# Kernel tuning notes

Hardware: AMD Instinct MI355X
Metric: run time of the kernel (lower is better)

Reference implementation:

```python
import jax, jax.numpy as jnp
import numpy as np

DIM = 512
HEADS = 8
AGENT = 49
POOL = 7  # int(sqrt(49))
EPS = 1e-5  # BatchNorm eps


def _adaptive_avg_pool(x, out_hw):
    # torch AdaptiveAvgPool2d semantics: bin i covers [floor(i*H/out), ceil((i+1)*H/out))
    B, C, H, W = x.shape
    cs = jnp.cumsum(jnp.cumsum(x, axis=2), axis=3)
    cs = jnp.pad(cs, ((0, 0), (0, 0), (1, 0), (1, 0)))  # integral image, [B,C,H+1,W+1]
    hs = np.floor(np.arange(out_hw) * H / out_hw).astype(np.int32)
    he = np.ceil((np.arange(out_hw) + 1) * H / out_hw).astype(np.int32)
    ws = np.floor(np.arange(out_hw) * W / out_hw).astype(np.int32)
    we = np.ceil((np.arange(out_hw) + 1) * W / out_hw).astype(np.int32)
    area = ((he - hs)[:, None] * (we - ws)[None, :]).astype(np.float32)
    s = (cs[:, :, he][:, :, :, we] - cs[:, :, hs][:, :, :, we]
         - cs[:, :, he][:, :, :, ws] + cs[:, :, hs][:, :, :, ws])
    return s / area


def setup_inputs() -> dict:
    key = jax.random.key(0)
    ks = jax.random.split(key, 8)
    d = DIM

    def w(k, shape, s=0.02):
        return jax.random.normal(k, shape, jnp.float32) * s

    return {
        "x": jax.random.normal(ks[0], (16, d, 32, 32), jnp.float32),
        "H": 32,
        "W": 32,
        "q_w": w(ks[1], (d, d)),
        "kv_w": w(ks[2], (2 * d, d)),
        "dw_w": w(ks[3], (d, 1, 3, 3), 0.1),   # depthwise 3x3, groups=d
        "dw_b": jnp.zeros((d,), jnp.float32),
        "bn_gamma": jnp.ones((d,), jnp.float32),
        "bn_beta": jnp.zeros((d,), jnp.float32),
        "bn_mean": jnp.zeros((d,), jnp.float32),
        "bn_var": jnp.ones((d,), jnp.float32),
        "pw_w": w(ks[4], (d, d, 1, 1)),          # pointwise 1x1 conv
        "pw_b": jnp.zeros((d,), jnp.float32),
        "proj_w": w(ks[5], (d, d)),
        "proj_b": jnp.zeros((d,), jnp.float32),
        "enh1_w": w(ks[6], (d, d)),
        "enh1_b": jnp.zeros((d,), jnp.float32),
        "enh2_w": w(ks[7], (d, d)),
        "enh2_b": jnp.zeros((d,), jnp.float32),
    }


def reference(x, H, W, q_w, kv_w, dw_w, dw_b, bn_gamma, bn_beta, bn_mean, bn_var,
              pw_w, pw_b, proj_w, proj_b, enh1_w, enh1_b, enh2_w, enh2_b):
    B, C, H, W = x.shape  # torch re-reads sizes from x
    N = H * W
    hd = C // HEADS
    scale = hd ** -0.5
    dn = ('NCHW', 'OIHW', 'NCHW')

    x_flat = x.reshape(B, C, N).transpose(0, 2, 1)            # [B,N,C]
    q = (x_flat @ q_w.T).reshape(B, N, HEADS, hd).transpose(0, 2, 1, 3)  # [B,h,N,hd]
    kv = (x_flat @ kv_w.T).reshape(B, N, 2, HEADS, hd).transpose(2, 0, 3, 1, 4)
    k, v = kv[0], kv[1]                                        # [B,h,N,hd]

    # agent tokens (faithful raw reshapes as in the torch code)
    a = _adaptive_avg_pool(x, POOL)                            # [B,C,7,7]
    a = a.reshape(B, C, AGENT).transpose(0, 2, 1)              # [B,49,C]
    a = a.reshape(B, C, POOL, POOL)                            # raw reshape (torch bug, kept)
    a = jax.lax.conv_general_dilated(a, dw_w, (1, 1), 'SAME',
                                     feature_group_count=C, dimension_numbers=dn)
    a = a + dw_b[None, :, None, None]
    a = (a - bn_mean[None, :, None, None]) * jax.lax.rsqrt(bn_var + EPS)[None, :, None, None]
    a = a * bn_gamma[None, :, None, None] + bn_beta[None, :, None, None]
    a = jax.nn.relu(a)
    a = jax.lax.conv_general_dilated(a, pw_w, (1, 1), 'SAME', dimension_numbers=dn)
    a = a + pw_b[None, :, None, None]
    a = a.reshape(B, AGENT, C)                                 # raw reshape
    a = a.reshape(B, HEADS, AGENT, hd)                         # raw reshape (torch bug, kept)

    # stage 1: agent <- kv
    agent_attn = jax.nn.softmax(jnp.einsum('bhad,bhnd->bhan', a, k) * scale, axis=-1)
    agg = jnp.einsum('bhan,bhnd->bhad', agent_attn, v)         # [B,h,49,hd]
    # stage 2: q <- agent
    q_attn = jax.nn.softmax(jnp.einsum('bhnd,bhad->bhna', q, a) * scale, axis=-1)
    enh = jnp.einsum('bhna,bhad->bhnd', q_attn, agg)           # [B,h,N,hd]
    enh = enh.transpose(0, 2, 1, 3).reshape(B, N, C)

    x_out = enh @ proj_w.T + proj_b
    out = (jax.nn.relu(x_out @ enh1_w.T + enh1_b) @ enh2_w.T + enh2_b) + x_out
    return out.reshape(B, C, H, W)  # raw reshape as in torch
```

## Files before the change

### kernel.cpp

```cpp
#include <hip/hip_runtime.h>
#include <stdint.h>


typedef float f32x4 __attribute__((ext_vector_type(4)));
typedef short s16x8 __attribute__((ext_vector_type(8)));

typedef __attribute__((address_space(1))) void glob_v;
typedef __attribute__((address_space(3))) void lds_v;
#define GLD16(g, l) \
  __builtin_amdgcn_global_load_lds((glob_v*)(g), (lds_v*)(l), 16, 0, 0)
#define VMCNT(N) asm volatile("s_waitcnt vmcnt(" #N ")" ::: "memory")
#define BAR() __builtin_amdgcn_s_barrier()

__device__ __forceinline__ float bf2f(unsigned short u) {
  union { unsigned int i; float f; } v; v.i = ((unsigned int)u) << 16; return v.f;
}
__device__ __forceinline__ unsigned short f2bf(float f) {
  union { float f; unsigned int i; } v; v.f = f;
  return (unsigned short)((v.i + 0x7FFFu + ((v.i >> 16) & 1u)) >> 16);
}

__constant__ int ws7[7] = {0, 4, 9, 13, 18, 22, 27};
__constant__ int we7[7] = {5, 10, 14, 19, 23, 28, 32};

__global__ __launch_bounds__(256) void k_transpose(const float* __restrict__ x,
                                                   unsigned short* __restrict__ xT,
                                                   float* __restrict__ p_rows) {
  __shared__ float tile[64][65];
  const int b = blockIdx.z, c0 = blockIdx.y * 64, n0 = blockIdx.x * 64;
  const int t = threadIdx.x, tn = t & 63, tg = t >> 6;
#pragma unroll
  for (int i = 0; i < 16; ++i) {
    const int c_l = tg * 16 + i;
    tile[c_l][tn] = x[(b * 512 + c0 + c_l) * 1024 + n0 + tn];
  }
  __syncthreads();
#pragma unroll
  for (int i = 0; i < 16; ++i) {
    const int n_l = tg * 16 + i;
    xT[(b * 1024 + n0 + n_l) * 512 + c0 + tn] = f2bf(tile[tn][n_l]);
  }
  if (t < 128) {
    const int c_l = t >> 1, rw = t & 1;
    const int rowg = blockIdx.x * 2 + rw;
    const float* src = &tile[c_l][rw * 32];
    float* dst = p_rows + ((b * 512 + c0 + c_l) * 32 + rowg) * 8;
#pragma unroll
    for (int jb = 0; jb < 7; ++jb) {
      float s = 0.f;
      for (int cc = ws7[jb]; cc < we7[jb]; ++cc) s += src[cc];
      dst[jb] = s;
    }
  }
}

__global__ __launch_bounds__(256) void k_poolred(const float* __restrict__ p_rows,
                                                 float* __restrict__ p) {
  const int u = blockIdx.x * 256 + threadIdx.x;
  if (u >= 401408) return;
  const int bc = u / 49, ij = u % 49;
  const int i = ij / 7, j = ij % 7;
  float s = 0.f;
  for (int r = ws7[i]; r < we7[i]; ++r) s += p_rows[bc * 256 + r * 8 + j];
  const float area = (float)((we7[i] - ws7[i]) * (we7[j] - ws7[j]));
  p[u] = s / area;
}

__global__ __launch_bounds__(256) void k_weights(
    const float* __restrict__ qw, const float* __restrict__ kvw,
    const float* __restrict__ pjw, const float* __restrict__ w1,
    const float* __restrict__ w2, unsigned short* __restrict__ Wqkv,
    unsigned short* __restrict__ Wpj, unsigned short* __restrict__ W1,
    unsigned short* __restrict__ W2) {
  const int u = blockIdx.x * 256 + threadIdx.x;
  const float* s; unsigned short* d; int su, du;
  if (u < 196608) { d = Wqkv; du = u;
    if (u < 65536) { s = qw; su = u; } else { s = kvw; su = u - 65536; } }
  else if (u < 262144) { s = pjw; su = u - 196608; d = Wpj; du = su; }
  else if (u < 327680) { s = w1; su = u - 262144; d = W1; du = su; }
  else { s = w2; su = u - 327680; d = W2; du = su; }
  const f32x4 val = ((const f32x4*)s)[su];
  uint2 pk;
  pk.x = (unsigned)f2bf(val[0]) | ((unsigned)f2bf(val[1]) << 16);
  pk.y = (unsigned)f2bf(val[2]) | ((unsigned)f2bf(val[3]) << 16);
  ((uint2*)d)[du] = pk;
}

__global__ __launch_bounds__(256) void k_dw(
    const float* __restrict__ p, const float* __restrict__ dww,
    const float* __restrict__ dwb, const float* __restrict__ g,
    const float* __restrict__ be, const float* __restrict__ mean,
    const float* __restrict__ var, float* __restrict__ r) {
  const int t = threadIdx.x, s = t & 63;
  if (s >= 49) return;
  const int bc = blockIdx.x * 4 + (t >> 6);
  const int b = bc >> 9, c = bc & 511;
  const int i = s / 7, j = s % 7;
  float sum = 0.f;
#pragma unroll
  for (int ki = 0; ki < 3; ++ki)
#pragma unroll
    for (int kj = 0; kj < 3; ++kj) {
      const int ii = i + ki - 1, jj = j + kj - 1;
      if (ii < 0 || ii > 6 || jj < 0 || jj > 6) continue;
      const int f = c * 49 + ii * 7 + jj;
      sum += dww[c * 9 + ki * 3 + kj] * p[(b * 512 + (f & 511)) * 49 + (f >> 9)];
    }
  sum += dwb[c];
  sum = (sum - mean[c]) * rsqrtf(var[c] + 1e-5f) * g[c] + be[c];
  r[bc * 49 + s] = fmaxf(sum, 0.f);
}

__global__ __launch_bounds__(256) void k_pw(const float* __restrict__ r,
                                            const float* __restrict__ w,
                                            const float* __restrict__ bias,
                                            float* __restrict__ A) {
  __shared__ float wl[128 * 36];
  __shared__ float rl[128 * 64];
  const int blk = blockIdx.x;
  const int b = blk >> 4, cg = blk & 15;
  const int t = threadIdx.x, wv = t >> 6, lane = t & 63;
  float acc[8];
#pragma unroll
  for (int j = 0; j < 8; ++j) acc[j] = 0.f;
  for (int ch = 0; ch < 4; ++ch) {
    __syncthreads();
#pragma unroll
    for (int u = t; u < 4096; u += 256) {
      const int co = u >> 7, ci = u & 127;
      wl[ci * 36 + co] = w[(cg * 32 + co) * 512 + ch * 128 + ci];
    }
    for (int u = t; u < 6272; u += 256) {
      const int ci = u / 49, s = u % 49;
      rl[ci * 64 + s] = r[b * 25088 + ch * 6272 + u];
    }
    __syncthreads();
#pragma unroll 4
    for (int ci = 0; ci < 128; ++ci) {
      const f32x4 w0 = *(const f32x4*)(wl + ci * 36 + wv * 8);
      const f32x4 w1 = *(const f32x4*)(wl + ci * 36 + wv * 8 + 4);
      const float rv = rl[ci * 64 + lane];
#pragma unroll
      for (int j = 0; j < 4; ++j) { acc[j] += w0[j] * rv; acc[4 + j] += w1[j] * rv; }
    }
  }
  if (lane < 49) {
#pragma unroll
    for (int j = 0; j < 8; ++j) {
      const int co = cg * 32 + wv * 8 + j;
      A[b * 25088 + co * 49 + lane] = acc[j] + bias[co];
    }
  }
}

template <int MODE>
__global__ __launch_bounds__(256) void k_gemm(
    const unsigned short* __restrict__ A, const unsigned short* __restrict__ B,
    unsigned short* __restrict__ oq, unsigned short* __restrict__ ok,
    unsigned short* __restrict__ ov, float* __restrict__ of,
    unsigned short* __restrict__ obf, const float* __restrict__ bias,
    const float* __restrict__ resid, float* __restrict__ dout) {
  __shared__ unsigned short As[3][4096];
  __shared__ unsigned short Bs[3][4096];
  const int t = threadIdx.x;
  constexpr int NB = (MODE == 0) ? 12 : 4;
  constexpr int NWG = NB * 128;
  const int swz = ((int)blockIdx.x & 7) * (NWG >> 3) + ((int)blockIdx.x >> 3);
  const int n0 = (swz % NB) * 128, m0 = (swz / NB) * 128;
  const int w = t >> 6, lane = t & 63;
  const int wr = w >> 1, wc = w & 1, lr = lane & 15, lg = lane >> 4;
  const unsigned short* gA = A + m0 * 512;
  const unsigned short* gB = B + n0 * 512;

  const int s_rp = t >> 3;
  const int s_g = (t & 7) ^ (s_rp & 7);
  const int s_r = (s_rp << 1) | (s_g >> 2);
  const int s_kq = (s_g & 3) * 8;
  auto stage = [&](int cur, int kt) {
    const int ko = kt * 32 + s_kq;
    GLD16(gA + s_r * 512 + ko, As[cur] + w * 512);
    GLD16(gA + (s_r + 64) * 512 + ko, As[cur] + 2048 + w * 512);
    GLD16(gB + s_r * 512 + ko, Bs[cur] + w * 512);
    GLD16(gB + (s_r + 64) * 512 + ko, Bs[cur] + 2048 + w * 512);
  };
  auto ldsw = [&](const unsigned short* hb, int rl, int lgq) -> s16x8 {
    const int rp = rl >> 1;
    const int gs = (((rl & 1) << 2) | lgq) ^ (rp & 7);
    return *(const s16x8*)(hb + rp * 64 + gs * 8);
  };

  f32x4 acc[4][4];
#pragma unroll
  for (int mi = 0; mi < 4; ++mi)
#pragma unroll
    for (int ni = 0; ni < 4; ++ni)
#pragma unroll
      for (int rr = 0; rr < 4; ++rr) acc[mi][ni][rr] = 0.f;

  stage(0, 0);
  stage(1, 1);
  for (int kt = 0; kt < 16; ++kt) {
    const int cur = kt % 3;
    if (kt < 14) {
      stage((kt + 2) % 3, kt + 2);
      VMCNT(8);
    } else if (kt == 14) {
      VMCNT(4);
    } else {
      VMCNT(0);
    }
    BAR();
    const unsigned short* Ah = As[cur] + wr * 2048;
    const unsigned short* Bh = Bs[cur] + wc * 2048;
    s16x8 af[4], bfr[4];
#pragma unroll
    for (int mi = 0; mi < 4; ++mi) af[mi] = ldsw(Ah, mi * 16 + lr, lg);
#pragma unroll
    for (int ni = 0; ni < 4; ++ni) bfr[ni] = ldsw(Bh, ni * 16 + lr, lg);
    __builtin_amdgcn_s_setprio(1);
#pragma unroll
    for (int mi = 0; mi < 4; ++mi)
#pragma unroll
      for (int ni = 0; ni < 4; ++ni)
        acc[mi][ni] = __builtin_amdgcn_mfma_f32_16x16x32_bf16(af[mi], bfr[ni],
                                                              acc[mi][ni], 0, 0, 0);
    __builtin_amdgcn_s_setprio(0);
    BAR();
  }

#pragma unroll
  for (int mi = 0; mi < 4; ++mi)
#pragma unroll
    for (int ni = 0; ni < 4; ++ni)
#pragma unroll
      for (int rr = 0; rr < 4; ++rr) {
        const int gm = m0 + wr * 64 + mi * 16 + lg * 4 + rr;
        const int gn = n0 + wc * 64 + ni * 16 + lr;
        const float val = acc[mi][ni][rr];
        if (MODE == 0) {
          const int b = gm >> 10, n = gm & 1023;
          const int hh = (gn >> 6) & 7, dd = gn & 63;
          const int idx = ((b * 8 + hh) * 1024 + n) * 64 + dd;
          const unsigned short bv = f2bf(val);
          if (gn < 512) oq[idx] = bv;
          else if (gn < 1024) ok[idx] = bv;
          else ov[idx] = bv;
        } else if (MODE == 1) {
          const float v2 = val + bias[gn];
          of[gm * 512 + gn] = v2;
          obf[gm * 512 + gn] = f2bf(v2);
        } else if (MODE == 2) {
          const float v2 = fmaxf(val + bias[gn], 0.f);
          obf[gm * 512 + gn] = f2bf(v2);
        } else {
          dout[gm * 512 + gn] = val + bias[gn] + resid[gm * 512 + gn];
        }
      }
}

__global__ __launch_bounds__(256) void k_aflash(
    const float* __restrict__ Abuf, const unsigned short* __restrict__ kbf,
    const unsigned short* __restrict__ vbf, float* __restrict__ numT,
    float* __restrict__ denG) {
  __shared__ unsigned short A_lds[64 * 72];
  __shared__ unsigned short K_lds[64 * 72];
  __shared__ unsigned short VT_lds[64 * 72];
  __shared__ unsigned short P_lds[64 * 72];
  const int blk = blockIdx.x;
  const int bh = blk >> 2, qtr = blk & 3;
  const int b = bh >> 3, h = bh & 7;
  const int t = threadIdx.x, w = t >> 6, lane = t & 63;
  const int lr = lane & 15, lg = lane >> 4;

  for (int u = t; u < 64 * 72; u += 256) A_lds[u] = 0;
  __syncthreads();
  for (int u = t; u < 3136; u += 256) {
    const int d = u / 49, ag = u % 49;
    A_lds[ag * 72 + d] = f2bf(Abuf[b * 25088 + (h * 64 + d) * 49 + ag]);
  }

  const unsigned short* kbase = kbf + bh * 65536 + qtr * 256 * 64;
  const unsigned short* vbase = vbf + bh * 65536 + qtr * 256 * 64;

  f32x4 num[4];
#pragma unroll
  for (int ni = 0; ni < 4; ++ni)
#pragma unroll
    for (int rr = 0; rr < 4; ++rr) num[ni][rr] = 0.f;
  float den[4] = {0.f, 0.f, 0.f, 0.f};

  for (int c = 0; c < 4; ++c) {
    const int n0 = c * 64;
    __syncthreads();
#pragma unroll
    for (int u = t; u < 512; u += 256) {
      const int rw = u >> 3, qq = u & 7;
      *(s16x8*)(K_lds + rw * 72 + qq * 8) =
          *(const s16x8*)(kbase + (n0 + rw) * 64 + qq * 8);
    }
#pragma unroll
    for (int u = t; u < 512; u += 256) {
      const int n_l = u & 63, qq = u >> 6;
      const s16x8 v = *(const s16x8*)(vbase + (n0 + n_l) * 64 + qq * 8);
#pragma unroll
      for (int j = 0; j < 8; ++j)
        VT_lds[(qq * 8 + j) * 72 + n_l] = (unsigned short)v[j];
    }
    __syncthreads();
    f32x4 s[4];
#pragma unroll
    for (int ni = 0; ni < 4; ++ni)
#pragma unroll
      for (int rr = 0; rr < 4; ++rr) s[ni][rr] = 0.f;
#pragma unroll
    for (int kk = 0; kk < 2; ++kk) {
      const s16x8 afr = *(const s16x8*)(A_lds + (w * 16 + lr) * 72 + kk * 32 + lg * 8);
#pragma unroll
      for (int ni = 0; ni < 4; ++ni) {
        const s16x8 bfr =
            *(const s16x8*)(K_lds + (ni * 16 + lr) * 72 + kk * 32 + lg * 8);
        s[ni] = __builtin_amdgcn_mfma_f32_16x16x32_bf16(afr, bfr, s[ni], 0, 0, 0);
      }
    }
#pragma unroll
    for (int ni = 0; ni < 4; ++ni)
#pragma unroll
      for (int rr = 0; rr < 4; ++rr) {
        const float p = __expf(s[ni][rr] * 0.125f);
        den[rr] += p;
        P_lds[(w * 16 + lg * 4 + rr) * 72 + ni * 16 + lr] = f2bf(p);
      }
#pragma unroll
    for (int kk = 0; kk < 2; ++kk) {
      const s16x8 pa = *(const s16x8*)(P_lds + (w * 16 + lr) * 72 + kk * 32 + lg * 8);
#pragma unroll
      for (int ni = 0; ni < 4; ++ni) {
        const s16x8 vfr =
            *(const s16x8*)(VT_lds + (ni * 16 + lr) * 72 + kk * 32 + lg * 8);
        num[ni] = __builtin_amdgcn_mfma_f32_16x16x32_bf16(pa, vfr, num[ni], 0, 0, 0);
      }
    }
  }
#pragma unroll
  for (int rr = 0; rr < 4; ++rr) {
#pragma unroll
    for (int o = 1; o < 16; o <<= 1) den[rr] += __shfl_xor(den[rr], o, 64);
  }
  const int obase = (qtr * 128 + bh) * 4096;
#pragma unroll
  for (int ni = 0; ni < 4; ++ni)
    *(f32x4*)(numT + obase + (ni * 16 + lr) * 64 + w * 16 + lg * 4) = num[ni];
  if (lr == 0) {
    f32x4 dv;
#pragma unroll
    for (int rr = 0; rr < 4; ++rr) dv[rr] = den[rr];
    *(f32x4*)(denG + (qtr * 128 + bh) * 64 + w * 16 + lg * 4) = dv;
  }
}

__global__ __launch_bounds__(256) void k_attn2(
    const float* __restrict__ Abuf, const float* __restrict__ numT,
    const float* __restrict__ denG, const unsigned short* __restrict__ qbf,
    unsigned short* __restrict__ enh) {
  __shared__ unsigned short A_lds[64 * 72];
  __shared__ unsigned short G_lds[64 * 72];
  __shared__ unsigned short P2_lds[4][64 * 72];
  __shared__ float den_lds[64];
  const int blk = blockIdx.x;
  const int bh = blk >> 2, nq = blk & 3;
  const int b = bh >> 3, h = bh & 7;
  const int t = threadIdx.x, w = t >> 6, lane = t & 63;
  const int lr = lane & 15, lg = lane >> 4;

  if (t < 64)
    den_lds[t] = 1.f / (denG[bh * 64 + t] + denG[8192 + bh * 64 + t] +
                        denG[16384 + bh * 64 + t] + denG[24576 + bh * 64 + t]);
  for (int u = t; u < 64 * 72; u += 256) A_lds[u] = 0;
  __syncthreads();
  for (int u = t; u < 3136; u += 256) {
    const int d = u / 49, ag = u % 49;
    A_lds[ag * 72 + d] = f2bf(Abuf[b * 25088 + (h * 64 + d) * 49 + ag]);
  }
  for (int u = t; u < 4096; u += 256) {
    const int d = u >> 6, ag = u & 63;
    const float v = (numT[bh * 4096 + u] + numT[524288 + bh * 4096 + u] +
                     numT[1048576 + bh * 4096 + u] + numT[1572864 + bh * 4096 + u]) *
                    den_lds[ag];
    G_lds[d * 72 + ag] = f2bf(v);
  }
  __syncthreads();

  const int nbase = nq * 256 + w * 64;
  const unsigned short* qp = qbf + (bh * 1024 + nbase) * 64;
  s16x8 qf[4][2];
#pragma unroll
  for (int mi = 0; mi < 4; ++mi)
#pragma unroll
    for (int kk = 0; kk < 2; ++kk)
      qf[mi][kk] = *(const s16x8*)(qp + (mi * 16 + lr) * 64 + kk * 32 + lg * 8);

  f32x4 L[4][4];
#pragma unroll
  for (int mi = 0; mi < 4; ++mi)
#pragma unroll
    for (int ni = 0; ni < 4; ++ni)
#pragma unroll
      for (int rr = 0; rr < 4; ++rr) L[mi][ni][rr] = 0.f;
#pragma unroll
  for (int kk = 0; kk < 2; ++kk)
#pragma unroll
    for (int ni = 0; ni < 4; ++ni) {
      const s16x8 bfr = *(const s16x8*)(A_lds + (ni * 16 + lr) * 72 + kk * 32 + lg * 8);
#pragma unroll
      for (int mi = 0; mi < 4; ++mi)
        L[mi][ni] = __builtin_amdgcn_mfma_f32_16x16x32_bf16(qf[mi][kk], bfr,
                                                            L[mi][ni], 0, 0, 0);
    }
  unsigned short* pw = P2_lds[w];
#pragma unroll
  for (int mi = 0; mi < 4; ++mi) {
    float ps[4][4];
    float rs[4];
#pragma unroll
    for (int rr = 0; rr < 4; ++rr) rs[rr] = 0.f;
#pragma unroll
    for (int ni = 0; ni < 4; ++ni) {
      const bool valid = (ni < 3) | (lr == 0);
#pragma unroll
      for (int rr = 0; rr < 4; ++rr) {
        const float p = valid ? __expf(L[mi][ni][rr] * 0.125f) : 0.f;
        ps[ni][rr] = p;
        rs[rr] += p;
      }
    }
#pragma unroll
    for (int rr = 0; rr < 4; ++rr) {
#pragma unroll
      for (int o = 1; o < 16; o <<= 1) rs[rr] += __shfl_xor(rs[rr], o, 64);
      rs[rr] = 1.f / rs[rr];
    }
#pragma unroll
    for (int ni = 0; ni < 4; ++ni)
#pragma unroll
      for (int rr = 0; rr < 4; ++rr)
        pw[(mi * 16 + lg * 4 + rr) * 72 + ni * 16 + lr] = f2bf(ps[ni][rr] * rs[rr]);
  }
#pragma unroll
  for (int mi = 0; mi < 4; ++mi) {
    f32x4 e[4];
#pragma unroll
    for (int ni = 0; ni < 4; ++ni)
#pragma unroll
      for (int rr = 0; rr < 4; ++rr) e[ni][rr] = 0.f;
#pragma unroll
    for (int kk = 0; kk < 2; ++kk) {
      const s16x8 pa = *(const s16x8*)(pw + (mi * 16 + lr) * 72 + kk * 32 + lg * 8);
#pragma unroll
      for (int ni = 0; ni < 4; ++ni) {
        const s16x8 gb = *(const s16x8*)(G_lds + (ni * 16 + lr) * 72 + kk * 32 + lg * 8);
        e[ni] = __builtin_amdgcn_mfma_f32_16x16x32_bf16(pa, gb, e[ni], 0, 0, 0);
      }
    }
#pragma unroll
    for (int ni = 0; ni < 4; ++ni)
#pragma unroll
      for (int rr = 0; rr < 4; ++rr) {
        const int n = nbase + mi * 16 + lg * 4 + rr;
        enh[(b * 1024 + n) * 512 + h * 64 + ni * 16 + lr] = f2bf(e[ni][rr]);
      }
  }
}

extern "C" void kernel_launch(void* const* d_in, const int* in_sizes, int n_in,
                              void* d_out, int out_size, void* d_ws, size_t ws_size,
                              hipStream_t stream) {
  const float* x    = (const float*)d_in[0];
  const float* q_w  = (const float*)d_in[3];
  const float* kv_w = (const float*)d_in[4];
  const float* dw_w = (const float*)d_in[5];
  const float* dw_b = (const float*)d_in[6];
  const float* bn_g = (const float*)d_in[7];
  const float* bn_b = (const float*)d_in[8];
  const float* bn_m = (const float*)d_in[9];
  const float* bn_v = (const float*)d_in[10];
  const float* pw_w = (const float*)d_in[11];
  const float* pw_b = (const float*)d_in[12];
  const float* pj_w = (const float*)d_in[13];
  const float* pj_b = (const float*)d_in[14];
  const float* e1_w = (const float*)d_in[15];
  const float* e1_b = (const float*)d_in[16];
  const float* e2_w = (const float*)d_in[17];
  const float* e2_b = (const float*)d_in[18];

  char* base = (char*)d_ws;
  size_t off = 0;
  auto alloc = [&](size_t bytes) -> void* {
    void* r = base + off;
    off += (bytes + 255) & ~(size_t)255;
    return r;
  };
  unsigned short* Wqkv = (unsigned short*)alloc(786432ull * 2);
  unsigned short* Wpj  = (unsigned short*)alloc(262144ull * 2);
  unsigned short* W1   = (unsigned short*)alloc(262144ull * 2);
  unsigned short* W2   = (unsigned short*)alloc(262144ull * 2);
  unsigned short* xT   = (unsigned short*)alloc(8388608ull * 2);
  unsigned short* qb   = (unsigned short*)alloc(8388608ull * 2);
  unsigned short* kb   = (unsigned short*)alloc(8388608ull * 2);
  unsigned short* vb   = (unsigned short*)alloc(8388608ull * 2);
  float* prow = (float*)alloc(2097152ull * 4);
  float* pbuf = (float*)alloc(401408ull * 4);
  float* rbuf = (float*)alloc(401408ull * 4);
  float* Abuf = (float*)alloc(401408ull * 4);
  float* numT = (float*)alloc(2097152ull * 4);
  float* denG = (float*)alloc(32768ull * 4);
  unsigned short* enh  = (unsigned short*)alloc(8388608ull * 2);
  float* xout = (float*)alloc(8388608ull * 4);
  unsigned short* xoutb = (unsigned short*)alloc(8388608ull * 2);
  unsigned short* h1    = (unsigned short*)alloc(8388608ull * 2);
  (void)ws_size; (void)in_sizes; (void)n_in; (void)out_size;

  k_weights<<<1536, 256, 0, stream>>>(q_w, kv_w, pj_w, e1_w, e2_w, Wqkv, Wpj, W1, W2);
  k_transpose<<<dim3(16, 8, 16), 256, 0, stream>>>(x, xT, prow);
  k_poolred<<<1568, 256, 0, stream>>>(prow, pbuf);
  k_dw<<<2048, 256, 0, stream>>>(pbuf, dw_w, dw_b, bn_g, bn_b, bn_m, bn_v, rbuf);
  k_pw<<<256, 256, 0, stream>>>(rbuf, pw_w, pw_b, Abuf);
  k_gemm<0><<<1536, 256, 0, stream>>>(xT, Wqkv, qb, kb, vb,
                                      nullptr, nullptr, nullptr, nullptr, nullptr);
  k_aflash<<<512, 256, 0, stream>>>(Abuf, kb, vb, numT, denG);
  k_attn2<<<512, 256, 0, stream>>>(Abuf, numT, denG, qb, enh);
  k_gemm<1><<<512, 256, 0, stream>>>(enh, Wpj, nullptr, nullptr, nullptr,
                                     xout, xoutb, pj_b, nullptr, nullptr);
  k_gemm<2><<<512, 256, 0, stream>>>(xoutb, W1, nullptr, nullptr, nullptr,
                                     nullptr, h1, e1_b, nullptr, nullptr);
  k_gemm<3><<<512, 256, 0, stream>>>(h1, W2, nullptr, nullptr, nullptr,
                                     nullptr, nullptr, e2_b, xout, (float*)d_out);
}
```

Baseline: 194.4 us.

## Merge weight cast into transpose, emit bf16 agent layout, precompute normalized aggregate

Fuses the weight bf16 conversion kernel into the transpose kernel as extra blocks, saving one launch. The pointwise conv now writes agent tokens directly as bf16 in the per-head [agent][dim] layout, so both attention kernels load them with vector copies instead of strided fp32 gathers and per-element conversion. A new small kernel reduces the partial numerators and denominators once per head and writes the normalized aggregate in bf16, replacing the four-fold redundant reduction in each attn2 block. This adds one launch and an extra buffer round-trip.

```diff
diff --git a/kernel.cpp b/kernel.cpp
--- a/kernel.cpp
+++ b/kernel.cpp
@@ -23,12 +23,33 @@
 __constant__ int ws7[7] = {0, 4, 9, 13, 18, 22, 27};
 __constant__ int we7[7] = {5, 10, 14, 19, 23, 28, 32};
 
-__global__ __launch_bounds__(256) void k_transpose(const float* __restrict__ x,
-                                                   unsigned short* __restrict__ xT,
-                                                   float* __restrict__ p_rows) {
+__global__ __launch_bounds__(256) void k_prep(
+    const float* __restrict__ x, unsigned short* __restrict__ xT,
+    float* __restrict__ p_rows, const float* __restrict__ qw,
+    const float* __restrict__ kvw, const float* __restrict__ pjw,
+    const float* __restrict__ w1, const float* __restrict__ w2,
+    unsigned short* __restrict__ Wqkv, unsigned short* __restrict__ Wpj,
+    unsigned short* __restrict__ W1, unsigned short* __restrict__ W2) {
+  const int bid = blockIdx.x, t = threadIdx.x;
+  if (bid >= 2048) {
+    const int u = (bid - 2048) * 256 + t;
+    const float* s; unsigned short* d; int su, du;
+    if (u < 196608) { d = Wqkv; du = u;
+      if (u < 65536) { s = qw; su = u; } else { s = kvw; su = u - 65536; } }
+    else if (u < 262144) { s = pjw; su = u - 196608; d = Wpj; du = su; }
+    else if (u < 327680) { s = w1; su = u - 262144; d = W1; du = su; }
+    else { s = w2; su = u - 327680; d = W2; du = su; }
+    const f32x4 val = ((const f32x4*)s)[su];
+    uint2 pk;
+    pk.x = (unsigned)f2bf(val[0]) | ((unsigned)f2bf(val[1]) << 16);
+    pk.y = (unsigned)f2bf(val[2]) | ((unsigned)f2bf(val[3]) << 16);
+    ((uint2*)d)[du] = pk;
+    return;
+  }
   __shared__ float tile[64][65];
-  const int b = blockIdx.z, c0 = blockIdx.y * 64, n0 = blockIdx.x * 64;
-  const int t = threadIdx.x, tn = t & 63, tg = t >> 6;
+  const int bx = bid & 15, by = (bid >> 4) & 7, bz = bid >> 7;
+  const int b = bz, c0 = by * 64, n0 = bx * 64;
+  const int tn = t & 63, tg = t >> 6;
 #pragma unroll
   for (int i = 0; i < 16; ++i) {
     const int c_l = tg * 16 + i;
@@ -42,7 +63,7 @@
   }
   if (t < 128) {
     const int c_l = t >> 1, rw = t & 1;
-    const int rowg = blockIdx.x * 2 + rw;
+    const int rowg = bx * 2 + rw;
     const float* src = &tile[c_l][rw * 32];
     float* dst = p_rows + ((b * 512 + c0 + c_l) * 32 + rowg) * 8;
 #pragma unroll
@@ -64,26 +85,6 @@
   for (int r = ws7[i]; r < we7[i]; ++r) s += p_rows[bc * 256 + r * 8 + j];
   const float area = (float)((we7[i] - ws7[i]) * (we7[j] - ws7[j]));
   p[u] = s / area;
-}
-
-__global__ __launch_bounds__(256) void k_weights(
-    const float* __restrict__ qw, const float* __restrict__ kvw,
-    const float* __restrict__ pjw, const float* __restrict__ w1,
-    const float* __restrict__ w2, unsigned short* __restrict__ Wqkv,
-    unsigned short* __restrict__ Wpj, unsigned short* __restrict__ W1,
-    unsigned short* __restrict__ W2) {
-  const int u = blockIdx.x * 256 + threadIdx.x;
-  const float* s; unsigned short* d; int su, du;
-  if (u < 196608) { d = Wqkv; du = u;
-    if (u < 65536) { s = qw; su = u; } else { s = kvw; su = u - 65536; } }
-  else if (u < 262144) { s = pjw; su = u - 196608; d = Wpj; du = su; }
-  else if (u < 327680) { s = w1; su = u - 262144; d = W1; du = su; }
-  else { s = w2; su = u - 327680; d = W2; du = su; }
-  const f32x4 val = ((const f32x4*)s)[su];
-  uint2 pk;
-  pk.x = (unsigned)f2bf(val[0]) | ((unsigned)f2bf(val[1]) << 16);
-  pk.y = (unsigned)f2bf(val[2]) | ((unsigned)f2bf(val[3]) << 16);
-  ((uint2*)d)[du] = pk;
 }
 
 __global__ __launch_bounds__(256) void k_dw(
@@ -114,7 +115,7 @@
 __global__ __launch_bounds__(256) void k_pw(const float* __restrict__ r,
                                             const float* __restrict__ w,
                                             const float* __restrict__ bias,
-                                            float* __restrict__ A) {
+                                            unsigned short* __restrict__ Abf) {
   __shared__ float wl[128 * 36];
   __shared__ float rl[128 * 64];
   const int blk = blockIdx.x;
@@ -145,11 +146,12 @@
     }
   }
   if (lane < 49) {
-#pragma unroll
-    for (int j = 0; j < 8; ++j) {
-      const int co = cg * 32 + wv * 8 + j;
-      A[b * 25088 + co * 49 + lane] = acc[j] + bias[co];
-    }
+    const int h = cg >> 1, d0 = (cg & 1) * 32 + wv * 8;
+    s16x8 pk;
+#pragma unroll
+    for (int j = 0; j < 8; ++j)
+      pk[j] = (short)f2bf(acc[j] + bias[cg * 32 + wv * 8 + j]);
+    *(s16x8*)(Abf + ((b * 8 + h) * 64 + lane) * 64 + d0) = pk;
   }
 }
 
@@ -259,7 +261,7 @@
 }
 
 __global__ __launch_bounds__(256) void k_aflash(
-    const float* __restrict__ Abuf, const unsigned short* __restrict__ kbf,
+    const unsigned short* __restrict__ Abf, const unsigned short* __restrict__ kbf,
     const unsigned short* __restrict__ vbf, float* __restrict__ numT,
     float* __restrict__ denG) {
   __shared__ unsigned short A_lds[64 * 72];
@@ -268,15 +270,14 @@
   __shared__ unsigned short P_lds[64 * 72];
   const int blk = blockIdx.x;
   const int bh = blk >> 2, qtr = blk & 3;
-  const int b = bh >> 3, h = bh & 7;
   const int t = threadIdx.x, w = t >> 6, lane = t & 63;
   const int lr = lane & 15, lg = lane >> 4;
 
   for (int u = t; u < 64 * 72; u += 256) A_lds[u] = 0;
   __syncthreads();
-  for (int u = t; u < 3136; u += 256) {
-    const int d = u / 49, ag = u % 49;
-    A_lds[ag * 72 + d] = f2bf(Abuf[b * 25088 + (h * 64 + d) * 49 + ag]);
+  for (int u = t; u < 392; u += 256) {
+    const int row = u >> 3, q = u & 7;
+    *(s16x8*)(A_lds + row * 72 + q * 8) = *(const s16x8*)(Abf + bh * 4096 + u * 8);
   }
 
   const unsigned short* kbase = kbf + bh * 65536 + qtr * 256 * 64;
@@ -358,35 +359,45 @@
   }
 }
 
+__global__ __launch_bounds__(256) void k_aggfin(const float* __restrict__ numT,
+                                                const float* __restrict__ denG,
+                                                unsigned short* __restrict__ Gbf) {
+  __shared__ float invden[64];
+  const int bh = blockIdx.x, t = threadIdx.x;
+  if (t < 64)
+    invden[t] = 1.f / (denG[bh * 64 + t] + denG[8192 + bh * 64 + t] +
+                       denG[16384 + bh * 64 + t] + denG[24576 + bh * 64 + t]);
+  __syncthreads();
+  for (int u = t; u < 4096; u += 256) {
+    const int ag = u & 63;
+    const float v = (numT[bh * 4096 + u] + numT[524288 + bh * 4096 + u] +
+                     numT[1048576 + bh * 4096 + u] + numT[1572864 + bh * 4096 + u]) *
+                    invden[ag];
+    Gbf[bh * 4096 + u] = f2bf(v);
+  }
+}
+
 __global__ __launch_bounds__(256) void k_attn2(
-    const float* __restrict__ Abuf, const float* __restrict__ numT,
-    const float* __restrict__ denG, const unsigned short* __restrict__ qbf,
-    unsigned short* __restrict__ enh) {
+    const unsigned short* __restrict__ Abf, const unsigned short* __restrict__ Gbf,
+    const unsigned short* __restrict__ qbf, unsigned short* __restrict__ enh) {
   __shared__ unsigned short A_lds[64 * 72];
   __shared__ unsigned short G_lds[64 * 72];
   __shared__ unsigned short P2_lds[4][64 * 72];
-  __shared__ float den_lds[64];
   const int blk = blockIdx.x;
   const int bh = blk >> 2, nq = blk & 3;
   const int b = bh >> 3, h = bh & 7;
   const int t = threadIdx.x, w = t >> 6, lane = t & 63;
   const int lr = lane & 15, lg = lane >> 4;
 
-  if (t < 64)
-    den_lds[t] = 1.f / (denG[bh * 64 + t] + denG[8192 + bh * 64 + t] +
-                        denG[16384 + bh * 64 + t] + denG[24576 + bh * 64 + t]);
   for (int u = t; u < 64 * 72; u += 256) A_lds[u] = 0;
   __syncthreads();
-  for (int u = t; u < 3136; u += 256) {
-    const int d = u / 49, ag = u % 49;
-    A_lds[ag * 72 + d] = f2bf(Abuf[b * 25088 + (h * 64 + d) * 49 + ag]);
-  }
-  for (int u = t; u < 4096; u += 256) {
-    const int d = u >> 6, ag = u & 63;
-    const float v = (numT[bh * 4096 + u] + numT[524288 + bh * 4096 + u] +
-                     numT[1048576 + bh * 4096 + u] + numT[1572864 + bh * 4096 + u]) *
-                    den_lds[ag];
-    G_lds[d * 72 + ag] = f2bf(v);
+  for (int u = t; u < 392; u += 256) {
+    const int row = u >> 3, q = u & 7;
+    *(s16x8*)(A_lds + row * 72 + q * 8) = *(const s16x8*)(Abf + bh * 4096 + u * 8);
+  }
+  for (int u = t; u < 512; u += 256) {
+    const int row = u >> 3, q = u & 7;
+    *(s16x8*)(G_lds + row * 72 + q * 8) = *(const s16x8*)(Gbf + bh * 4096 + u * 8);
   }
   __syncthreads();
 
@@ -510,24 +521,26 @@
   float* prow = (float*)alloc(2097152ull * 4);
   float* pbuf = (float*)alloc(401408ull * 4);
   float* rbuf = (float*)alloc(401408ull * 4);
-  float* Abuf = (float*)alloc(401408ull * 4);
+  unsigned short* Abf = (unsigned short*)alloc(524288ull * 2);
   float* numT = (float*)alloc(2097152ull * 4);
   float* denG = (float*)alloc(32768ull * 4);
+  unsigned short* Gbf = (unsigned short*)alloc(524288ull * 2);
   unsigned short* enh  = (unsigned short*)alloc(8388608ull * 2);
   float* xout = (float*)alloc(8388608ull * 4);
   unsigned short* xoutb = (unsigned short*)alloc(8388608ull * 2);
   unsigned short* h1    = (unsigned short*)alloc(8388608ull * 2);
   (void)ws_size; (void)in_sizes; (void)n_in; (void)out_size;
 
-  k_weights<<<1536, 256, 0, stream>>>(q_w, kv_w, pj_w, e1_w, e2_w, Wqkv, Wpj, W1, W2);
-  k_transpose<<<dim3(16, 8, 16), 256, 0, stream>>>(x, xT, prow);
+  k_prep<<<3584, 256, 0, stream>>>(x, xT, prow, q_w, kv_w, pj_w, e1_w, e2_w,
+                                   Wqkv, Wpj, W1, W2);
   k_poolred<<<1568, 256, 0, stream>>>(prow, pbuf);
   k_dw<<<2048, 256, 0, stream>>>(pbuf, dw_w, dw_b, bn_g, bn_b, bn_m, bn_v, rbuf);
-  k_pw<<<256, 256, 0, stream>>>(rbuf, pw_w, pw_b, Abuf);
+  k_pw<<<256, 256, 0, stream>>>(rbuf, pw_w, pw_b, Abf);
   k_gemm<0><<<1536, 256, 0, stream>>>(xT, Wqkv, qb, kb, vb,
                                       nullptr, nullptr, nullptr, nullptr, nullptr);
-  k_aflash<<<512, 256, 0, stream>>>(Abuf, kb, vb, numT, denG);
-  k_attn2<<<512, 256, 0, stream>>>(Abuf, numT, denG, qb, enh);
+  k_aflash<<<512, 256, 0, stream>>>(Abf, kb, vb, numT, denG);
+  k_aggfin<<<128, 256, 0, stream>>>(numT, denG, Gbf);
+  k_attn2<<<512, 256, 0, stream>>>(Abf, Gbf, qb, enh);
   k_gemm<1><<<512, 256, 0, stream>>>(enh, Wpj, nullptr, nullptr, nullptr,
                                      xout, xoutb, pj_b, nullptr, nullptr);
   k_gemm<2><<<512, 256, 0, stream>>>(xoutb, W1, nullptr, nullptr, nullptr,
```

Result: faster. 187.3 us (-3.6%).
